# Kernel tuning notes

Hardware: AMD Instinct MI355X
Metric: run time of the kernel (lower is better)

## Reference

```python
import jax, jax.numpy as jnp
import numpy as np

B, N, DIM = 2, 4096, 1024
HEADS, DH, W = 16, 64, 512
INNER = int(DIM * 2 * 4 / 3)  # 2730 (GEGLU FeedForward, mult=4)


def setup_inputs() -> dict:
    key = jax.random.key(0)
    ks = jax.random.split(key, 6)
    rn = lambda k, shape, sc: jax.random.normal(k, shape, jnp.float32) * sc
    return {
        "x": rn(ks[0], (B, N, DIM), 1.0),
        "ln1_w": jnp.ones((DIM,), jnp.float32),
        "ln1_b": jnp.zeros((DIM,), jnp.float32),
        "w_qkv": rn(ks[1], (DIM, 3 * HEADS * DH), 0.02),
        "w_out": rn(ks[2], (HEADS * DH, DIM), 0.02),
        "ln2_w": jnp.ones((DIM,), jnp.float32),
        "w_ff1": rn(ks[3], (DIM, 2 * INNER), 0.02),
        "w_ff2": rn(ks[4], (INNER, DIM), 0.02),
    }


def _layernorm(x, w, b=None, eps=1e-5):
    m = x.mean(-1, keepdims=True)
    v = x.var(-1, keepdims=True)
    y = (x - m) * jax.lax.rsqrt(v + eps) * w
    return y + b if b is not None else y


def _rotary_freqs(n, d):
    inv = 1.0 / (10000.0 ** (jnp.arange(0, d, 2, dtype=jnp.float32) / d))
    f = jnp.arange(n, dtype=jnp.float32)[:, None] * inv[None, :]  # [n, d/2]
    return jnp.concatenate([f, f], axis=-1)  # [n, d]


def _rotate_half(x):
    x1, x2 = jnp.split(x, 2, axis=-1)
    return jnp.concatenate([-x2, x1], axis=-1)


def _apply_rotary(x, freqs):
    return x * jnp.cos(freqs) + _rotate_half(x) * jnp.sin(freqs)


def reference(x, ln1_w, ln1_b, w_qkv, w_out, ln2_w, w_ff1, w_ff2):
    # ---- LocalMHA (prenorm, causal windowed attention, look_backward=1) ----
    h = _layernorm(x, ln1_w, ln1_b)
    qkv = h @ w_qkv  # [b, n, 3*h*d]
    q, k, v = jnp.split(qkv, 3, axis=-1)
    to_heads = lambda t: t.reshape(B, N, HEADS, DH).transpose(0, 2, 1, 3)  # [b,h,n,d]
    q, k, v = map(to_heads, (q, k, v))

    freqs = _rotary_freqs(N, DH)  # [n, d]
    q = _apply_rotary(q, freqs)
    k = _apply_rotary(k, freqs)
    q = q * (DH ** -0.5)

    nw = N // W
    bq = q.reshape(B, HEADS, nw, W, DH)
    bk = k.reshape(B, HEADS, nw, W, DH)
    bv = v.reshape(B, HEADS, nw, W, DH)

    def look_back(t):  # prepend previous window (zeros for first window)
        prev = jnp.concatenate([jnp.zeros_like(t[:, :, :1]), t[:, :, :-1]], axis=2)
        return jnp.concatenate([prev, t], axis=3)  # [b,h,nw,2w,d]

    kk, vv = look_back(bk), look_back(bv)

    tq = jnp.arange(N).reshape(nw, W)
    tprev = jnp.concatenate([jnp.full((1, W), -1, tq.dtype), tq[:-1]], axis=0)
    tk = jnp.concatenate([tprev, tq], axis=1)  # [nw, 2w]
    mask = (tq[:, :, None] >= tk[:, None, :]) & (tk[:, None, :] >= 0)  # causal + pad

    sim = jnp.einsum('bhnqd,bhnkd->bhnqk', bq, kk)
    sim = jnp.where(mask, sim, jnp.finfo(sim.dtype).min / 2)
    attn = jax.nn.softmax(sim, axis=-1)
    o = jnp.einsum('bhnqk,bhnkd->bhnqd', attn, vv)
    o = o.reshape(B, HEADS, N, DH).transpose(0, 2, 1, 3).reshape(B, N, HEADS * DH)
    x = o @ w_out + x  # residual

    # ---- FeedForward: LN(gamma only) -> GEGLU -> Linear, residual ----
    h = _layernorm(x, ln2_w)
    u = h @ w_ff1
    a, g = jnp.split(u, 2, axis=-1)
    x = (a * jax.nn.gelu(g, approximate=False)) @ w_ff2 + x
    return x
```

## Files before the change

kernel.cpp:

```cpp
#include <hip/hip_runtime.h>
#include <stdint.h>

typedef unsigned short u16;
typedef unsigned int u32;

#define BATCH 2
#define NSEQ  4096
#define DIM   1024
#define HEADS 16
#define DH    64
#define WIN   512
#define INNER 2730
#define ROWS  8192
#define QKV_N 3072
#define FF1_N 5460
#define FF1_NP 5632
#define INNER_P 2816
#define KROT 0.28782313663f

typedef __attribute__((ext_vector_type(8))) short short8;
typedef __attribute__((ext_vector_type(4))) float float4v;

__device__ __forceinline__ float bf2f(u16 u){ union{u32 i;float f;}c; c.i=((u32)u)<<16; return c.f; }
__device__ __forceinline__ u16 f2bf(float f){ union{float f;u32 i;}c; c.f=f; u32 i=c.i;
    return (u16)((i + 0x7FFFu + ((i>>16)&1u))>>16); }

__device__ __forceinline__ float gelu_fast(float g) {
    float t = 0.7978845608f * (g + 0.044715f * g * g * g);
    float th = 1.f - 2.f / (1.f + __expf(2.f * t));
    return 0.5f * g * (1.f + th);
}

__device__ __forceinline__ void gl_lds16(const u16* g, const u16* ldsbase) {
    __builtin_amdgcn_global_load_lds(
        (const __attribute__((address_space(1))) u32*)(uintptr_t)g,
        (__attribute__((address_space(3))) u32*)(uintptr_t)ldsbase,
        16, 0, 0);
}

__device__ __forceinline__ int ff1_src(int n, bool& ok) {
    int t = n >> 7, m = n & 127, j = m >> 4, l = m & 15;
    int p = t * 64 + ((j >> 1) << 4) + l;
    ok = (p < INNER);
    return (j & 1) ? (INNER + p) : p;
}

template <bool REMAP>
__global__ __launch_bounds__(256) void wtrans_kernel(const float* __restrict__ w, u16* __restrict__ wt,
                                                     int K0, int N0, int K1, int N1) {
    __shared__ float tile[32][33];
    int kt = blockIdx.x, nt = blockIdx.y;
    int tx = threadIdx.x & 31, ty = threadIdx.x >> 5;
    int nl = nt * 32 + tx;
    bool ok = (nl < N1);
    int sc = nl;
    if (REMAP) { bool v; sc = ff1_src(nl < N1 ? nl : 0, v); ok = ok && v; }
    else ok = ok && (nl < N0);
#pragma unroll
    for (int yy = 0; yy < 4; yy++) {
        int k = kt*32 + ty + yy*8;
        tile[ty+yy*8][tx] = (k < K0 && ok) ? w[(size_t)k*N0 + sc] : 0.f;
    }
    __syncthreads();
#pragma unroll
    for (int yy = 0; yy < 4; yy++) {
        int n = nt*32 + ty + yy*8, k = kt*32 + tx;
        if (n < N1 && k < K1) wt[(size_t)n*K1 + k] = f2bf(tile[tx][ty+yy*8]);
    }
}

__global__ __launch_bounds__(256) void ln_kernel(const float* __restrict__ x,
                                                 const float* __restrict__ w,
                                                 const float* __restrict__ b,
                                                 u16* __restrict__ out) {
    int row = blockIdx.x;
    const float* xr = x + (size_t)row * DIM;
    int t = threadIdx.x;
    float v[4];
    float s = 0.f, s2 = 0.f;
#pragma unroll
    for (int i = 0; i < 4; i++) {
        float f = xr[t + 256 * i];
        v[i] = f; s += f; s2 += f * f;
    }
#pragma unroll
    for (int off = 32; off; off >>= 1) { s += __shfl_xor(s, off); s2 += __shfl_xor(s2, off); }
    __shared__ float ls[10];
    int wave = t >> 6, lane = t & 63;
    if (lane == 0) { ls[wave] = s; ls[4 + wave] = s2; }
    __syncthreads();
    if (t == 0) {
        float ts  = ls[0] + ls[1] + ls[2] + ls[3];
        float ts2 = ls[4] + ls[5] + ls[6] + ls[7];
        float mean = ts * (1.f / DIM);
        float var  = ts2 * (1.f / DIM) - mean * mean;
        ls[8] = mean; ls[9] = 1.f / sqrtf(var + 1e-5f);
    }
    __syncthreads();
    float mean = ls[8], inv = ls[9];
    u16* orow = out + (size_t)row * DIM;
#pragma unroll
    for (int i = 0; i < 4; i++) {
        int c = t + 256 * i;
        float y = (v[i] - mean) * inv * w[c];
        if (b) y += b[c];
        orow[c] = f2bf(y);
    }
}

template <int MODE, int PHASED>
__global__ __launch_bounds__(512, 2) void gemm256(const u16* __restrict__ A,
                                                  const u16* __restrict__ Bt,
                                                  void* __restrict__ Cv,
                                                  int N, int K) {
    extern __shared__ u16 lds[];
    u16* Asm = lds;
    u16* Bsm = lds + 4 * 8192;
    int tiles_n = N >> 8;
    int gs  = tiles_n << 3;
    int gid = blockIdx.x / gs;
    int loc = blockIdx.x % gs;
    int tm = gid * 8 + (loc & 7);
    int tn = loc >> 3;
    int tid = threadIdx.x, wave = tid >> 6, lane = tid & 63;
    int quad = lane >> 4, l15 = lane & 15;
    int wm = wave >> 2, wn = wave & 3;
    int srow = wave * 16 + (lane >> 2);
    int sgrp = (lane & 3) ^ ((srow >> 1) & 3);
    const u16* Ag = A  + (size_t)(tm * 256 + srow) * K + sgrp * 8;
    const u16* Bg = Bt + (size_t)(tn * 256 + srow) * K + sgrp * 8;
    u16* Asw = Asm + wave * 512;
    u16* Bsw = Bsm + wave * 512;
    int rg = (l15 >> 1) & 3;
    int nk = K >> 5;

    float4v acc[8][4];
#pragma unroll
    for (int i = 0; i < 8; i++)
#pragma unroll
        for (int j = 0; j < 4; j++) acc[i][j] = (float4v){0.f, 0.f, 0.f, 0.f};

    auto stage2 = [&](int t, int h) {
        int b = t & 3;
        int k0 = t << 5;
        if (h == 0) {
            gl_lds16(Ag + k0,                   Asw + b * 8192);
            gl_lds16(Ag + (size_t)128 * K + k0, Asw + b * 8192 + 4096);
        } else {
            gl_lds16(Bg + k0,                   Bsw + b * 8192);
            gl_lds16(Bg + (size_t)128 * K + k0, Bsw + b * 8192 + 4096);
        }
    };
    auto ldsA = [&](int t, int i) -> short8 {
        const u16* Ab = Asm + (t & 3) * 8192;
        return *(const short8*)&Ab[(wm*128 + i*16 + l15) * 32 + ((quad ^ rg) * 8)];
    };
    auto ldsB = [&](int t, int j) -> short8 {
        const u16* Bb = Bsm + (t & 3) * 8192;
        return *(const short8*)&Bb[(wn*64 + j*16 + l15) * 32 + ((quad ^ rg) * 8)];
    };

    stage2(0, 0); stage2(0, 1);
    stage2(1, 0); stage2(1, 1);
    stage2(2, 0); stage2(2, 1);

    if (PHASED == 0) {
        auto compute = [&](int t) {
            short8 af[8], bfr[4];
#pragma unroll
            for (int i = 0; i < 8; i++) af[i] = ldsA(t, i);
#pragma unroll
            for (int j = 0; j < 4; j++) bfr[j] = ldsB(t, j);
            __builtin_amdgcn_s_setprio(1);
#pragma unroll
            for (int i = 0; i < 8; i++)
#pragma unroll
                for (int j = 0; j < 4; j++)
                    acc[i][j] = __builtin_amdgcn_mfma_f32_16x16x32_bf16(af[i], bfr[j], acc[i][j], 0, 0, 0);
            __builtin_amdgcn_s_setprio(0);
        };
#define KSTEP(T, VM) \
        asm volatile("s_waitcnt vmcnt(" #VM ")" ::: "memory"); \
        __builtin_amdgcn_s_barrier(); \
        __builtin_amdgcn_sched_barrier(0); \
        compute(T); \
        if ((T) + 3 < nk) { stage2((T) + 3, 0); stage2((T) + 3, 1); }
        for (int t = 0; t < nk - 2; ++t) { KSTEP(t, 8); }
        { KSTEP(nk - 2, 4); }
        { KSTEP(nk - 1, 0); }
#undef KSTEP
    } else {
        asm volatile("s_waitcnt vmcnt(8)" ::: "memory");
        __builtin_amdgcn_s_barrier();
        for (int t = 0; t < nk; ++t) {
            short8 af[8], bfr[4];
#pragma unroll
            for (int i = 0; i < 4; i++) af[i] = ldsA(t, i);
#pragma unroll
            for (int j = 0; j < 4; j++) bfr[j] = ldsB(t, j);
            if (t + 3 < nk) stage2(t + 3, 0);
            __builtin_amdgcn_s_setprio(1);
#pragma unroll
            for (int i = 0; i < 4; i++)
#pragma unroll
                for (int j = 0; j < 4; j++)
                    acc[i][j] = __builtin_amdgcn_mfma_f32_16x16x32_bf16(af[i], bfr[j], acc[i][j], 0, 0, 0);
            __builtin_amdgcn_s_setprio(0);
            __builtin_amdgcn_s_barrier();
#pragma unroll
            for (int i = 4; i < 8; i++) af[i] = ldsA(t, i);
            if (t + 3 < nk) stage2(t + 3, 1);
            __builtin_amdgcn_s_setprio(1);
#pragma unroll
            for (int i = 4; i < 8; i++)
#pragma unroll
                for (int j = 0; j < 4; j++)
                    acc[i][j] = __builtin_amdgcn_mfma_f32_16x16x32_bf16(af[i], bfr[j], acc[i][j], 0, 0, 0);
            __builtin_amdgcn_s_setprio(0);
            if (t < nk - 1) {
                if (t < nk - 3)       asm volatile("s_waitcnt vmcnt(8)" ::: "memory");
                else if (t == nk - 3) asm volatile("s_waitcnt vmcnt(4)" ::: "memory");
                else                  asm volatile("s_waitcnt vmcnt(0)" ::: "memory");
                __builtin_amdgcn_s_barrier();
            }
        }
    }

    if (MODE == 2) {
        u16* C = (u16*)Cv;
        int sector = tn >> 2;
        if (sector < 2) {
            float inv0 = __expf(-(float)l15 * KROT);
            float inv1 = __expf(-(float)(l15 + 16) * KROT);
            float sc = (sector == 0) ? 0.125f : 1.0f;
#pragma unroll
            for (int i = 0; i < 8; i++) {
#pragma unroll
                for (int r = 0; r < 4; r++) {
                    int row = tm*256 + wm*128 + i*16 + quad*4 + r;
                    float fn = (float)(row & (NSEQ - 1));
                    float s0, c0, s1, c1;
                    __sincosf(fn * inv0, &s0, &c0);
                    __sincosf(fn * inv1, &s1, &c1);
                    float a0 = acc[i][0][r], a1 = acc[i][1][r];
                    float a2 = acc[i][2][r], a3 = acc[i][3][r];
                    size_t base = (size_t)row * N + tn*256 + wn*64 + l15;
                    C[base]      = f2bf((a0*c0 - a2*s0) * sc);
                    C[base + 16] = f2bf((a1*c1 - a3*s1) * sc);
                    C[base + 32] = f2bf((a2*c0 + a0*s0) * sc);
                    C[base + 48] = f2bf((a3*c1 + a1*s1) * sc);
                }
            }
        } else {
#pragma unroll
            for (int i = 0; i < 8; i++)
#pragma unroll
                for (int r = 0; r < 4; r++) {
                    size_t base = (size_t)(tm*256 + wm*128 + i*16 + quad*4 + r) * N + tn*256 + wn*64 + l15;
#pragma unroll
                    for (int j = 0; j < 4; j++) C[base + j*16] = f2bf(acc[i][j][r]);
                }
        }
        return;
    }
    if (MODE == 3) {
        u16* ag = (u16*)Cv;
        int t128 = tn * 2 + (wn >> 1);
        int cb = t128 * 64 + (wn & 1) * 32;
#pragma unroll
        for (int i = 0; i < 8; i++) {
#pragma unroll
            for (int r = 0; r < 4; r++) {
                size_t row = (size_t)(tm*256 + wm*128 + i*16 + quad*4 + r);
#pragma unroll
                for (int jp = 0; jp < 2; jp++) {
                    float a = acc[i][2*jp][r];
                    float g = acc[i][2*jp+1][r];
                    int col = cb + jp*16 + l15;
                    ag[row * INNER_P + col] = f2bf(a * gelu_fast(g));
                }
            }
        }
        return;
    }
}

__global__ __launch_bounds__(256, 2) void gemm_mn128(const u16* __restrict__ A,
                                                     const u16* __restrict__ Bt,
                                                     const float* __restrict__ resid,
                                                     float* __restrict__ C,
                                                     int N, int K) {
    extern __shared__ u16 lds[];
    int x = blockIdx.x & 7, s5 = blockIdx.x >> 3;
    int tm = x * 4 + (s5 & 3);
    int tn = s5 >> 2;
    int tid = threadIdx.x, wave = tid >> 6, lane = tid & 63;
    int quad = lane >> 4, l15 = lane & 15;
    int wm = wave >> 1, wn = wave & 1;
    int rg = (l15 >> 1) & 3;
    int srA = wave * 64 + (lane >> 2);
    int srB = wave * 32 + (lane >> 2);
    const u16* AgB = A  + (size_t)(tm * 256) * K;
    const u16* BgB = Bt + (size_t)(tn * 128) * K;
    int nk = K >> 5;

    float4v acc[8][4];
#pragma unroll
    for (int i = 0; i < 8; i++)
#pragma unroll
        for (int j = 0; j < 4; j++) acc[i][j] = (float4v){0.f, 0.f, 0.f, 0.f};

    auto stage = [&](int t) {
        int s = t % 3;
        int k0 = t << 5;
        u16* As = lds + s * 12288;
        u16* Bs = lds + s * 12288 + 8192;
#pragma unroll
        for (int q = 0; q < 4; q++) {
            int row = srA + q * 16;
            int g = (lane & 3) ^ ((row >> 1) & 3);
            gl_lds16(AgB + (size_t)row * K + k0 + g * 8, As + wave * 2048 + q * 512);
        }
#pragma unroll
        for (int q = 0; q < 2; q++) {
            int row = srB + q * 16;
            int g = (lane & 3) ^ ((row >> 1) & 3);
            gl_lds16(BgB + (size_t)row * K + k0 + g * 8, Bs + wave * 1024 + q * 512);
        }
    };

    stage(0); stage(1);
    for (int t = 0; t < nk; ++t) {
        if (t < nk - 1) asm volatile("s_waitcnt vmcnt(6)" ::: "memory");
        else            asm volatile("s_waitcnt vmcnt(0)" ::: "memory");
        __builtin_amdgcn_s_barrier();
        __builtin_amdgcn_sched_barrier(0);
        {
            int s = t % 3;
            const u16* As = lds + s * 12288;
            const u16* Bs = lds + s * 12288 + 8192;
            short8 af[8], bfr[4];
#pragma unroll
            for (int i = 0; i < 8; i++)
                af[i] = *(const short8*)&As[(wm*128 + i*16 + l15) * 32 + ((quad ^ rg) * 8)];
#pragma unroll
            for (int j = 0; j < 4; j++)
                bfr[j] = *(const short8*)&Bs[(wn*64 + j*16 + l15) * 32 + ((quad ^ rg) * 8)];
            __builtin_amdgcn_s_setprio(1);
#pragma unroll
            for (int i = 0; i < 8; i++)
#pragma unroll
                for (int j = 0; j < 4; j++)
                    acc[i][j] = __builtin_amdgcn_mfma_f32_16x16x32_bf16(af[i], bfr[j], acc[i][j], 0, 0, 0);
            __builtin_amdgcn_s_setprio(0);
        }
        if (t + 2 < nk) stage(t + 2);
    }

#pragma unroll
    for (int i = 0; i < 8; i++) {
#pragma unroll
        for (int r = 0; r < 4; r++) {
            size_t row = (size_t)(tm*256 + wm*128 + i*16 + quad*4 + r);
#pragma unroll
            for (int j = 0; j < 4; j++) {
                int col = tn*128 + wn*64 + j*16 + l15;
                size_t idx = row * N + col;
                C[idx] = acc[i][j][r] + resid[idx];
            }
        }
    }
}

__global__ __launch_bounds__(256) void vtrans_kernel(const u16* __restrict__ qkv, u16* __restrict__ vt) {
    __shared__ u16 tile[64][72];
    int t = threadIdx.x;
    int n0 = (blockIdx.x & 63) * 64;
    int hh = (blockIdx.x >> 6) & 15;
    int b  = blockIdx.x >> 10;
    int r = t >> 2, cb = (t & 3) * 16;
    const u16* src = qkv + (size_t)(b * NSEQ + n0 + r) * QKV_N + 2 * DIM + hh * 64 + cb;
    uint4 v0 = *(const uint4*)(src);
    uint4 v1 = *(const uint4*)(src + 8);
    *(uint4*)&tile[r][cb]     = v0;
    *(uint4*)&tile[r][cb + 8] = v1;
    __syncthreads();
    int d = t >> 2, nb = (t & 3) * 16;
    __align__(16) u16 vals[16];
#pragma unroll
    for (int e = 0; e < 16; e++) vals[e] = tile[nb + e][d];
    u16* dst = vt + ((size_t)(b * HEADS + hh) * DH + d) * NSEQ + n0 + nb;
    *(uint4*)(dst)     = *(uint4*)&vals[0];
    *(uint4*)(dst + 8) = *(uint4*)&vals[8];
}

__global__ __launch_bounds__(256) void attn_kernel(const u16* __restrict__ qkv,
                                                   const u16* __restrict__ vt,
                                                   u16* __restrict__ o) {
    __shared__ u16 Ks[128 * 64];
    __shared__ u16 Vs[64 * 128];
    __shared__ u16 p_lds[4][16][136];
    int tid = threadIdx.x, wave = tid >> 6, lane = tid & 63;
    int quad = lane >> 4, l15 = lane & 15;
    int bi = blockIdx.x;
    int qb = bi & 7, w0 = (bi >> 3) & 7, hh = (bi >> 6) & 15, b = bi >> 10;
    int qt = qb * 4 + wave;
    int qlocal = qt * 16 + l15;
    const u16* qp = qkv + (size_t)(b*NSEQ + w0*WIN + qt*16 + l15) * QKV_N + hh*64 + quad*8;
    short8 bq0 = *(const short8*)(qp);
    short8 bq1 = *(const short8*)(qp + 32);
    int krow0 = b * NSEQ + (w0 - 1) * WIN;
    const u16* vbase = vt + (size_t)(b * HEADS + hh) * DH * NSEQ + (w0 - 1) * WIN;
    int ks_row = lane >> 3;
    int ks_g   = (lane & 7) ^ ks_row;
    int vs_row = lane >> 4;
    int vs_j0  = lane & 15;
    int swz = l15 & 7;
    float m_ = -1e30f, l_ = 0.f;
    float4v O[4] = {{0,0,0,0},{0,0,0,0},{0,0,0,0},{0,0,0,0}};
    int cstart = (w0 == 0) ? 4 : 0;
    int clast  = (512 + qb * 64 + 63) >> 7;
    u16 (*pt)[136] = p_lds[wave];
    for (int c = cstart; c <= clast; c++) {
        int kb = c * 128;
        __syncthreads();
#pragma unroll
        for (int i = 0; i < 4; i++) {
            int kloc = wave * 32 + i * 8 + ks_row;
            gl_lds16(qkv + (size_t)(krow0 + kb + kloc) * QKV_N + DIM + hh*64 + ks_g*8,
                     &Ks[(wave*32 + i*8) * 64]);
        }
#pragma unroll
        for (int i = 0; i < 4; i++) {
            int dloc = wave * 16 + i * 4 + vs_row;
            int jsrc = vs_j0 ^ (dloc & 7);
            gl_lds16(vbase + (size_t)dloc * NSEQ + kb + jsrc * 8,
                     &Vs[(wave*16 + i*4) * 128]);
        }
        __syncthreads();
        float4v s[8];
#pragma unroll
        for (int t = 0; t < 8; t++) {
            int krow = (t*16 + l15) * 64;
            short8 ka0 = *(const short8*)&Ks[krow + ((quad    ) ^ swz) * 8];
            short8 ka1 = *(const short8*)&Ks[krow + ((quad + 4) ^ swz) * 8];
            float4v st = {0.f, 0.f, 0.f, 0.f};
            st = __builtin_amdgcn_mfma_f32_16x16x32_bf16(ka0, bq0, st, 0, 0, 0);
            st = __builtin_amdgcn_mfma_f32_16x16x32_bf16(ka1, bq1, st, 0, 0, 0);
            int ck = kb + t*16 + quad*4;
#pragma unroll
            for (int r = 0; r < 4; r++)
                if (ck + r >= 512 && ck + r - 512 > qlocal) st[r] = -1e30f;
            s[t] = st;
        }
        float mc = -1e30f;
#pragma unroll
        for (int t = 0; t < 8; t++)
#pragma unroll
            for (int r = 0; r < 4; r++) mc = fmaxf(mc, s[t][r]);
        mc = fmaxf(mc, __shfl_xor(mc, 16));
        mc = fmaxf(mc, __shfl_xor(mc, 32));
        float mn = fmaxf(m_, mc);
        float alpha = __expf(m_ - mn);
        m_ = mn;
        float su = 0.f;
#pragma unroll
        for (int t = 0; t < 8; t++) {
            union { u16 h[4]; uint2 v; } pk;
#pragma unroll
            for (int r = 0; r < 4; r++) {
                float p = __expf(s[t][r] - mn);
                su += p;
                pk.h[r] = f2bf(p);
            }
            *(uint2*)&pt[l15][t*16 + quad*4] = pk.v;
        }
        su += __shfl_xor(su, 16);
        su += __shfl_xor(su, 32);
        l_ = l_ * alpha + su;
#pragma unroll
        for (int t = 0; t < 4; t++)
#pragma unroll
            for (int r = 0; r < 4; r++) O[t][r] *= alpha;
#pragma unroll
        for (int g = 0; g < 4; g++) {
            short8 pf = *(const short8*)&pt[l15][g*32 + quad*8];
#pragma unroll
            for (int t = 0; t < 4; t++) {
                short8 vf = *(const short8*)&Vs[(t*16 + l15) * 128 + ((g*4 + quad) ^ swz) * 8];
                O[t] = __builtin_amdgcn_mfma_f32_16x16x32_bf16(vf, pf, O[t], 0, 0, 0);
            }
        }
    }
    float inv = 1.f / l_;
    u16* op = o + (size_t)(b*NSEQ + w0*WIN + qt*16 + l15) * DIM + hh*64;
#pragma unroll
    for (int t = 0; t < 4; t++) {
        union { u16 h[4]; uint2 v; } pk;
#pragma unroll
        for (int r = 0; r < 4; r++) pk.h[r] = f2bf(O[t][r] * inv);
        *(uint2*)(op + t*16 + quad*4) = pk.v;
    }
}

extern "C" void kernel_launch(void* const* d_in, const int* in_sizes, int n_in,
                              void* d_out, int out_size, void* d_ws, size_t ws_size,
                              hipStream_t stream) {
    const float* x      = (const float*)d_in[0];
    const float* ln1_w  = (const float*)d_in[1];
    const float* ln1_b  = (const float*)d_in[2];
    const float* w_qkv  = (const float*)d_in[3];
    const float* w_out  = (const float*)d_in[4];
    const float* ln2_w  = (const float*)d_in[5];
    const float* w_ff1  = (const float*)d_in[6];
    const float* w_ff2  = (const float*)d_in[7];
    float* out = (float*)d_out;

    static bool cfg = false;
    if (!cfg) {
        hipFuncSetAttribute((const void*)gemm256<2, 0>, hipFuncAttributeMaxDynamicSharedMemorySize, 131072);
        hipFuncSetAttribute((const void*)gemm256<3, 1>, hipFuncAttributeMaxDynamicSharedMemorySize, 131072);
        hipFuncSetAttribute((const void*)gemm_mn128,    hipFuncAttributeMaxDynamicSharedMemorySize, 73728);
        cfg = true;
    }

    char* ws = (char*)d_ws;
    size_t off = 0;
    auto alloc = [&](size_t bytes) { size_t o = off; off += (bytes + 255) & ~(size_t)255; return o; };
    size_t off_wqt  = alloc((size_t)QKV_N  * DIM * 2);
    size_t off_wot  = alloc((size_t)DIM    * DIM * 2);
    size_t off_wf1t = alloc((size_t)FF1_NP * DIM * 2);
    size_t off_wf2t = alloc((size_t)DIM    * INNER_P * 2);
    size_t off_h    = alloc((size_t)ROWS * DIM * 2);
    size_t sz_qkv = (size_t)ROWS * QKV_N * 2;
    size_t sz_vt  = (size_t)BATCH * HEADS * DH * NSEQ * 2;
    size_t off_qkv  = alloc(sz_qkv);
    size_t off_vt   = alloc(sz_vt);
    size_t off_o    = alloc((size_t)ROWS * DIM * 2);
    size_t off_x1   = alloc((size_t)ROWS * DIM * 4);
    size_t off_ag   = alloc((size_t)ROWS * INNER_P * 2);

    u16* wqt  = (u16*)(ws + off_wqt);
    u16* wot  = (u16*)(ws + off_wot);
    u16* wf1t = (u16*)(ws + off_wf1t);
    u16* wf2t = (u16*)(ws + off_wf2t);
    u16* h    = (u16*)(ws + off_h);
    u16* qkv  = (u16*)(ws + off_qkv);
    u16* vt   = (u16*)(ws + off_vt);
    u16* o    = (u16*)(ws + off_o);
    float* x1 = (float*)(ws + off_x1);
    u16* ag   = (u16*)(ws + off_ag);

    wtrans_kernel<false><<<dim3(32, 96),  256, 0, stream>>>(w_qkv, wqt,  DIM,   QKV_N, DIM,     QKV_N);
    wtrans_kernel<false><<<dim3(32, 32),  256, 0, stream>>>(w_out, wot,  DIM,   DIM,   DIM,     DIM);
    wtrans_kernel<true ><<<dim3(32, 176), 256, 0, stream>>>(w_ff1, wf1t, DIM,   FF1_N, DIM,     FF1_NP);
    wtrans_kernel<false><<<dim3(88, 32),  256, 0, stream>>>(w_ff2, wf2t, INNER, DIM,   INNER_P, DIM);

    ln_kernel<<<ROWS, 256, 0, stream>>>(x, ln1_w, ln1_b, h);
    gemm256<2, 0><<<(ROWS/256) * (QKV_N/256), 512, 131072, stream>>>(h, wqt, qkv, QKV_N, DIM);
    vtrans_kernel<<<BATCH * HEADS * (NSEQ / 64), 256, 0, stream>>>(qkv, vt);
    attn_kernel<<<BATCH * HEADS * 8 * 8, 256, 0, stream>>>(qkv, vt, o);
    gemm_mn128<<<256, 256, 73728, stream>>>(o, wot, x, x1, DIM, DIM);
    ln_kernel<<<ROWS, 256, 0, stream>>>(x1, ln2_w, nullptr, h);
    gemm256<3, 1><<<(ROWS/256) * (FF1_NP/256), 512, 131072, stream>>>(h, wf1t, ag, FF1_NP, DIM);
    gemm_mn128<<<256, 256, 73728, stream>>>(ag, wf2t, x1, out, DIM, INNER_P);

    (void)in_sizes; (void)n_in; (void)out_size; (void)ws_size;
}
```

Measured before the change: 527.4 us.

## Replace 256x256 GEMM tiles with 128x256 tiles and 3-stage LDS pipeline

The QKV and FF1 GEMMs drop from a 512-thread 256x256 block tile with a 4-deep LDS ring to a 256-thread 128x256 tile with a 3-stage ring using 72KB of LDS. The separate phased variant for FF1 is removed and both modes share one simpler loop. This doubles the grid size and lowers LDS use per block, aiming to improve wave scheduling and occupancy. The cost is less operand reuse per block, since each block now covers half as many A rows for the same B tile, and a shallower prefetch depth.

Measured after the change: 510.5 us. -3.2%, faster.

```diff
diff --git a/kernel.cpp b/kernel.cpp
--- a/kernel.cpp
+++ b/kernel.cpp
@@ -108,14 +108,12 @@
     }
 }
 
-template <int MODE, int PHASED>
-__global__ __launch_bounds__(512, 2) void gemm256(const u16* __restrict__ A,
-                                                  const u16* __restrict__ Bt,
-                                                  void* __restrict__ Cv,
-                                                  int N, int K) {
+template <int MODE>
+__global__ __launch_bounds__(256, 2) void gemm_k(const u16* __restrict__ A,
+                                                 const u16* __restrict__ Bt,
+                                                 void* __restrict__ Cv,
+                                                 int N, int K) {
     extern __shared__ u16 lds[];
-    u16* Asm = lds;
-    u16* Bsm = lds + 4 * 8192;
     int tiles_n = N >> 8;
     int gs  = tiles_n << 3;
     int gid = blockIdx.x / gs;
@@ -124,14 +122,12 @@
     int tn = loc >> 3;
     int tid = threadIdx.x, wave = tid >> 6, lane = tid & 63;
     int quad = lane >> 4, l15 = lane & 15;
-    int wm = wave >> 2, wn = wave & 3;
-    int srow = wave * 16 + (lane >> 2);
-    int sgrp = (lane & 3) ^ ((srow >> 1) & 3);
-    const u16* Ag = A  + (size_t)(tm * 256 + srow) * K + sgrp * 8;
-    const u16* Bg = Bt + (size_t)(tn * 256 + srow) * K + sgrp * 8;
-    u16* Asw = Asm + wave * 512;
-    u16* Bsw = Bsm + wave * 512;
+    int wn = wave;
     int rg = (l15 >> 1) & 3;
+    int srA = wave * 32 + (lane >> 2);
+    int srB = wave * 64 + (lane >> 2);
+    const u16* AgB = A  + (size_t)(tm * 128) * K;
+    const u16* BgB = Bt + (size_t)(tn * 256) * K;
     int nk = K >> 5;
 
     float4v acc[8][4];
@@ -140,37 +136,42 @@
 #pragma unroll
         for (int j = 0; j < 4; j++) acc[i][j] = (float4v){0.f, 0.f, 0.f, 0.f};
 
-    auto stage2 = [&](int t, int h) {
-        int b = t & 3;
+    auto stage = [&](int t) {
+        int s = t % 3;
         int k0 = t << 5;
-        if (h == 0) {
-            gl_lds16(Ag + k0,                   Asw + b * 8192);
-            gl_lds16(Ag + (size_t)128 * K + k0, Asw + b * 8192 + 4096);
-        } else {
-            gl_lds16(Bg + k0,                   Bsw + b * 8192);
-            gl_lds16(Bg + (size_t)128 * K + k0, Bsw + b * 8192 + 4096);
+        u16* As = lds + s * 12288;
+        u16* Bs = lds + s * 12288 + 4096;
+#pragma unroll
+        for (int q = 0; q < 2; q++) {
+            int row = srA + q * 16;
+            int g = (lane & 3) ^ ((row >> 1) & 3);
+            gl_lds16(AgB + (size_t)row * K + k0 + g * 8, As + wave * 1024 + q * 512);
+        }
+#pragma unroll
+        for (int q = 0; q < 4; q++) {
+            int row = srB + q * 16;
+            int g = (lane & 3) ^ ((row >> 1) & 3);
+            gl_lds16(BgB + (size_t)row * K + k0 + g * 8, Bs + wave * 2048 + q * 512);
         }
     };
-    auto ldsA = [&](int t, int i) -> short8 {
-        const u16* Ab = Asm + (t & 3) * 8192;
-        return *(const short8*)&Ab[(wm*128 + i*16 + l15) * 32 + ((quad ^ rg) * 8)];
-    };
-    auto ldsB = [&](int t, int j) -> short8 {
-        const u16* Bb = Bsm + (t & 3) * 8192;
-        return *(const short8*)&Bb[(wn*64 + j*16 + l15) * 32 + ((quad ^ rg) * 8)];
-    };
-
-    stage2(0, 0); stage2(0, 1);
-    stage2(1, 0); stage2(1, 1);
-    stage2(2, 0); stage2(2, 1);
-
-    if (PHASED == 0) {
-        auto compute = [&](int t) {
+
+    stage(0); stage(1);
+    for (int t = 0; t < nk; ++t) {
+        if (t < nk - 1) asm volatile("s_waitcnt vmcnt(6)" ::: "memory");
+        else            asm volatile("s_waitcnt vmcnt(0)" ::: "memory");
+        __builtin_amdgcn_s_barrier();
+        __builtin_amdgcn_sched_barrier(0);
+        {
+            int s = t % 3;
+            const u16* As = lds + s * 12288;
+            const u16* Bs = lds + s * 12288 + 4096;
             short8 af[8], bfr[4];
 #pragma unroll
-            for (int i = 0; i < 8; i++) af[i] = ldsA(t, i);
-#pragma unroll
-            for (int j = 0; j < 4; j++) bfr[j] = ldsB(t, j);
+            for (int i = 0; i < 8; i++)
+                af[i] = *(const short8*)&As[(i*16 + l15) * 32 + ((quad ^ rg) * 8)];
+#pragma unroll
+            for (int j = 0; j < 4; j++)
+                bfr[j] = *(const short8*)&Bs[(wn*64 + j*16 + l15) * 32 + ((quad ^ rg) * 8)];
             __builtin_amdgcn_s_setprio(1);
 #pragma unroll
             for (int i = 0; i < 8; i++)
@@ -178,52 +179,8 @@
                 for (int j = 0; j < 4; j++)
                     acc[i][j] = __builtin_amdgcn_mfma_f32_16x16x32_bf16(af[i], bfr[j], acc[i][j], 0, 0, 0);
             __builtin_amdgcn_s_setprio(0);
-        };
-#define KSTEP(T, VM) \
-        asm volatile("s_waitcnt vmcnt(" #VM ")" ::: "memory"); \
-        __builtin_amdgcn_s_barrier(); \
-        __builtin_amdgcn_sched_barrier(0); \
-        compute(T); \
-        if ((T) + 3 < nk) { stage2((T) + 3, 0); stage2((T) + 3, 1); }
-        for (int t = 0; t < nk - 2; ++t) { KSTEP(t, 8); }
-        { KSTEP(nk - 2, 4); }
-        { KSTEP(nk - 1, 0); }
-#undef KSTEP
-    } else {
-        asm volatile("s_waitcnt vmcnt(8)" ::: "memory");
-        __builtin_amdgcn_s_barrier();
-        for (int t = 0; t < nk; ++t) {
-            short8 af[8], bfr[4];
-#pragma unroll
-            for (int i = 0; i < 4; i++) af[i] = ldsA(t, i);
-#pragma unroll
-            for (int j = 0; j < 4; j++) bfr[j] = ldsB(t, j);
-            if (t + 3 < nk) stage2(t + 3, 0);
-            __builtin_amdgcn_s_setprio(1);
-#pragma unroll
-            for (int i = 0; i < 4; i++)
-#pragma unroll
-                for (int j = 0; j < 4; j++)
-                    acc[i][j] = __builtin_amdgcn_mfma_f32_16x16x32_bf16(af[i], bfr[j], acc[i][j], 0, 0, 0);
-            __builtin_amdgcn_s_setprio(0);
-            __builtin_amdgcn_s_barrier();
-#pragma unroll
-            for (int i = 4; i < 8; i++) af[i] = ldsA(t, i);
-            if (t + 3 < nk) stage2(t + 3, 1);
-            __builtin_amdgcn_s_setprio(1);
-#pragma unroll
-            for (int i = 4; i < 8; i++)
-#pragma unroll
-                for (int j = 0; j < 4; j++)
-                    acc[i][j] = __builtin_amdgcn_mfma_f32_16x16x32_bf16(af[i], bfr[j], acc[i][j], 0, 0, 0);
-            __builtin_amdgcn_s_setprio(0);
-            if (t < nk - 1) {
-                if (t < nk - 3)       asm volatile("s_waitcnt vmcnt(8)" ::: "memory");
-                else if (t == nk - 3) asm volatile("s_waitcnt vmcnt(4)" ::: "memory");
-                else                  asm volatile("s_waitcnt vmcnt(0)" ::: "memory");
-                __builtin_amdgcn_s_barrier();
-            }
-        }
+        }
+        if (t + 2 < nk) stage(t + 2);
     }
 
     if (MODE == 2) {
@@ -237,7 +194,7 @@
             for (int i = 0; i < 8; i++) {
 #pragma unroll
                 for (int r = 0; r < 4; r++) {
-                    int row = tm*256 + wm*128 + i*16 + quad*4 + r;
+                    int row = tm*128 + i*16 + quad*4 + r;
                     float fn = (float)(row & (NSEQ - 1));
                     float s0, c0, s1, c1;
                     __sincosf(fn * inv0, &s0, &c0);
@@ -256,7 +213,7 @@
             for (int i = 0; i < 8; i++)
 #pragma unroll
                 for (int r = 0; r < 4; r++) {
-                    size_t base = (size_t)(tm*256 + wm*128 + i*16 + quad*4 + r) * N + tn*256 + wn*64 + l15;
+                    size_t base = (size_t)(tm*128 + i*16 + quad*4 + r) * N + tn*256 + wn*64 + l15;
 #pragma unroll
                     for (int j = 0; j < 4; j++) C[base + j*16] = f2bf(acc[i][j][r]);
                 }
@@ -271,7 +228,7 @@
         for (int i = 0; i < 8; i++) {
 #pragma unroll
             for (int r = 0; r < 4; r++) {
-                size_t row = (size_t)(tm*256 + wm*128 + i*16 + quad*4 + r);
+                size_t row = (size_t)(tm*128 + i*16 + quad*4 + r);
 #pragma unroll
                 for (int jp = 0; jp < 2; jp++) {
                     float a = acc[i][2*jp][r];
@@ -518,9 +475,9 @@
 
     static bool cfg = false;
     if (!cfg) {
-        hipFuncSetAttribute((const void*)gemm256<2, 0>, hipFuncAttributeMaxDynamicSharedMemorySize, 131072);
-        hipFuncSetAttribute((const void*)gemm256<3, 1>, hipFuncAttributeMaxDynamicSharedMemorySize, 131072);
-        hipFuncSetAttribute((const void*)gemm_mn128,    hipFuncAttributeMaxDynamicSharedMemorySize, 73728);
+        hipFuncSetAttribute((const void*)gemm_k<2>,  hipFuncAttributeMaxDynamicSharedMemorySize, 73728);
+        hipFuncSetAttribute((const void*)gemm_k<3>,  hipFuncAttributeMaxDynamicSharedMemorySize, 73728);
+        hipFuncSetAttribute((const void*)gemm_mn128, hipFuncAttributeMaxDynamicSharedMemorySize, 73728);
         cfg = true;
     }
 
@@ -557,12 +514,12 @@
     wtrans_kernel<false><<<dim3(88, 32),  256, 0, stream>>>(w_ff2, wf2t, INNER, DIM,   INNER_P, DIM);
 
     ln_kernel<<<ROWS, 256, 0, stream>>>(x, ln1_w, ln1_b, h);
-    gemm256<2, 0><<<(ROWS/256) * (QKV_N/256), 512, 131072, stream>>>(h, wqt, qkv, QKV_N, DIM);
+    gemm_k<2><<<(ROWS/128) * (QKV_N/256), 256, 73728, stream>>>(h, wqt, qkv, QKV_N, DIM);
     vtrans_kernel<<<BATCH * HEADS * (NSEQ / 64), 256, 0, stream>>>(qkv, vt);
     attn_kernel<<<BATCH * HEADS * 8 * 8, 256, 0, stream>>>(qkv, vt, o);
     gemm_mn128<<<256, 256, 73728, stream>>>(o, wot, x, x1, DIM, DIM);
     ln_kernel<<<ROWS, 256, 0, stream>>>(x1, ln2_w, nullptr, h);
-    gemm256<3, 1><<<(ROWS/256) * (FF1_NP/256), 512, 131072, stream>>>(h, wf1t, ag, FF1_NP, DIM);
+    gemm_k<3><<<(ROWS/128) * (FF1_NP/256), 256, 73728, stream>>>(h, wf1t, ag, FF1_NP, DIM);
     gemm_mn128<<<256, 256, 73728, stream>>>(ag, wf2t, x1, out, DIM, INNER_P);
 
     (void)in_sizes; (void)n_in; (void)out_size; (void)ws_size;
```
